# Performance work log

Hardware: AMD Instinct MI355X
Metric: run time of the kernel (lower is better)

The kernel has to match this reference:

```python
import jax, jax.numpy as jnp
import numpy as np

N, E = 20000, 320000
CUR, HID, OUT, H = 256, 256, 64, 6  # cur_dim, hidden_dim, output_dim, gat heads


def setup_inputs() -> dict:
    key = jax.random.key(0)
    ks = jax.random.split(key, 16)
    p = lambda k, shape: jax.random.normal(k, shape, jnp.float32) * 0.05
    return dict(
        x=jax.random.normal(ks[0], (N, CUR), jnp.float32),
        edge_index=jax.random.randint(ks[1], (2, E), 0, N),
        edge_weight=jax.random.uniform(ks[2], (E,), jnp.float32),
        Wp=p(ks[3], (CUR, HID)), bp=p(ks[4], (HID,)),
        W_gat=p(ks[5], (HID, H * OUT)),
        att_src=p(ks[6], (H, OUT)), att_dst=p(ks[7], (H, OUT)),
        b_gat=p(ks[8], (H * OUT,)),
        W_gcn0=p(ks[9], (HID, OUT)), b_gcn0=p(ks[10], (OUT,)),
        W_gcn1=p(ks[11], (HID, OUT)), b_gcn1=p(ks[12], (OUT,)),
        W_arma_init=p(ks[13], (H * OUT, OUT)),
        W_arma_root=p(ks[14], (H * OUT, OUT)),
        b_arma=p(ks[15], (OUT,)),
    )


def _seg_sum(v, ids, n):
    return jax.ops.segment_sum(v, ids, num_segments=n)


def _gat(h, src, dst, W, a_s, a_d, b):
    # PyG GATConv: add self loops, per-edge attention, softmax over incoming edges.
    n = h.shape[0]
    loops = jnp.arange(n)
    s = jnp.concatenate([src, loops])
    d = jnp.concatenate([dst, loops])
    xw = (h @ W).reshape(n, H, OUT)               # [N,H,F]
    al = (xw * a_s).sum(-1)                       # [N,H] source term
    ar = (xw * a_d).sum(-1)                       # [N,H] target term
    e = jax.nn.leaky_relu(al[s] + ar[d], 0.2)     # [E',H]
    m = jax.ops.segment_max(e, d, num_segments=n)  # stable softmax per target
    pe = jnp.exp(e - m[d])
    alpha = pe / _seg_sum(pe, d, n)[d]
    out = _seg_sum(alpha[:, :, None] * xw[s], d, n)  # [N,H,F]
    return out.reshape(n, H * OUT) + b


def _gcn(h, src, dst, w, W, b):
    # PyG GCNConv: self loops (weight 1), symmetric D^-1/2 A D^-1/2 normalization.
    n = h.shape[0]
    loops = jnp.arange(n)
    s = jnp.concatenate([src, loops])
    d = jnp.concatenate([dst, loops])
    w2 = jnp.concatenate([w, jnp.ones((n,), h.dtype)])
    deg = _seg_sum(w2, d, n)
    dinv = jnp.where(deg > 0, jax.lax.rsqrt(deg), 0.0)
    norm = dinv[s] * w2 * dinv[d]
    xw = h @ W
    return _seg_sum(norm[:, None] * xw[s], d, n) + b


def _arma(h, src, dst, w, Wi, Wr, b):
    # PyG ARMAConv, num_stacks=1, num_layers=1, act=ReLU; gcn_norm WITHOUT self loops.
    n = h.shape[0]
    deg = _seg_sum(w, dst, n)
    dinv = jnp.where(deg > 0, jax.lax.rsqrt(deg), 0.0)
    norm = dinv[src] * w * dinv[dst]
    t = h @ Wi
    agg = _seg_sum(norm[:, None] * t[src], dst, n)
    return jax.nn.relu(agg + h @ Wr + b)


def reference(x, edge_index, edge_weight, Wp, bp, W_gat, att_src, att_dst, b_gat,
              W_gcn0, b_gcn0, W_gcn1, b_gcn1, W_arma_init, W_arma_root, b_arma):
    src, dst = edge_index[0], edge_index[1]
    h = x @ Wp + bp
    lrelu = lambda v: jax.nn.leaky_relu(v, 0.01)  # F.leaky_relu default slope
    h1 = lrelu(_gat(h, src, dst, W_gat, att_src, att_dst, b_gat))   # [N, 6*64]
    h2 = lrelu(_gcn(h, src, dst, edge_weight, W_gcn0, b_gcn0))       # [N, 64]
    h3 = lrelu(_gcn(h, src, dst, edge_weight, W_gcn1, b_gcn1))       # [N, 64]
    h4 = lrelu(_arma(h1, src, dst, edge_weight, W_arma_init, W_arma_root, b_arma))
    return jnp.tanh(jnp.concatenate([h1, h2, h3, h4], axis=1))      # [N, 576]
```

## Files before the change

### kernel.cpp

```cpp
#include <hip/hip_runtime.h>


#define NN 20000
#define EE 320000
#define GATD 384
#define NH 6
#define OUTD 64
#define ODIM 576

typedef __bf16 bf16_8 __attribute__((ext_vector_type(8)));
typedef float f32_4 __attribute__((ext_vector_type(4)));

__device__ __forceinline__ float lrelu(float x, float s) { return x > 0.f ? x : s * x; }

__device__ __forceinline__ float loadf(const void* p, size_t i, int f32) {
  return f32 ? ((const float*)p)[i] : (float)((const __bf16*)p)[i];
}

struct ProbeArgs {
  const void* ptr[15];
  int cnt[15];
  int flagidx[15];
  const int* ei;
};
__global__ void k_probe_all(ProbeArgs a, int* __restrict__ flags) {
  __shared__ int cnt;
  if (threadIdx.x == 0) cnt = 0;
  __syncthreads();
  int b = blockIdx.x;
  if (b < 15) {
    const unsigned short* u = (const unsigned short*)a.ptr[b];
    int m = a.cnt[b] < 2048 ? a.cnt[b] : 2048;
    int c = 0;
    for (int i = threadIdx.x; i < m; i += 256) {
      float v = __uint_as_float(((unsigned int)u[i]) << 16);
      if (!(fabsf(v) < 1e4f)) c++;
    }
    if (c) atomicAdd(&cnt, c);
    __syncthreads();
    if (threadIdx.x == 0) flags[a.flagidx[b]] = (cnt > m / 16) ? 1 : 0;
  } else {
    int c = 0;
    for (int i = threadIdx.x; i < 1024; i += 256)
      if (a.ei[2 * i + 1] != 0) c++;
    if (c) atomicAdd(&cnt, c);
    __syncthreads();
    if (threadIdx.x == 0) flags[16] = (cnt <= 2) ? 1 : 0;
  }
}

struct CvtSeg { const void* in; __bf16* out; int n; int flagidx; int blk0; };
struct CvtArgs { CvtSeg s[7]; };
struct TSeg { const void* in; __bf16* out; int R; int C; int flagidx; int blk0; };
struct TArgs { TSeg s[6]; };
__global__ void k_cvt_merged(CvtArgs ca, int ncvtblk, TArgs ta, const int* __restrict__ flags) {
  if ((int)blockIdx.x < ncvtblk) {
    int b = blockIdx.x;
    int k = 0;
    while (k + 1 < 7 && ca.s[k + 1].blk0 <= b) k++;
    const CvtSeg sg = ca.s[k];
    int i = (b - sg.blk0) * 256 + threadIdx.x;
    if (i >= sg.n) return;
    sg.out[i] = flags[sg.flagidx] ? (__bf16)((const float*)sg.in)[i] : ((const __bf16*)sg.in)[i];
    return;
  }
  __shared__ float t[32][33];
  int b = blockIdx.x - ncvtblk;
  int k = 0;
  while (k + 1 < 6 && ta.s[k + 1].blk0 <= b) k++;
  const TSeg sg = ta.s[k];
  int f32 = flags[sg.flagidx];
  int tpx = (sg.C + 31) >> 5;
  int lt = b - sg.blk0;
  int c0 = (lt % tpx) * 32, r0 = (lt / tpx) * 32;
  int tid = threadIdx.x;
  for (int idx = tid; idx < 1024; idx += 256) {
    int r = idx >> 5, c = idx & 31;
    if (r0 + r < sg.R && c0 + c < sg.C)
      t[r][c] = loadf(sg.in, (size_t)(r0 + r) * sg.C + (c0 + c), f32);
  }
  __syncthreads();
  for (int idx = tid; idx < 1024; idx += 256) {
    int r = idx >> 5, c = idx & 31;
    if (c0 + r < sg.C && r0 + c < sg.R)
      sg.out[(size_t)(c0 + r) * sg.R + (r0 + c)] = (__bf16)t[c][r];
  }
}

__global__ void k_count(const int* __restrict__ ei, const void* __restrict__ ew,
                        const int* __restrict__ flags,
                        int* __restrict__ deg, float* __restrict__ wdeg) {
  int e = blockIdx.x * 256 + threadIdx.x;
  if (e >= EE) return;
  int sh = flags[16];
  int d = ei[(size_t)(EE + e) << sh];
  atomicAdd(&deg[d], 1);
  atomicAdd(&wdeg[d], loadf(ew, e, flags[2]));
}

__global__ __launch_bounds__(256) void k_scan1(const int* __restrict__ deg,
                                               int* __restrict__ bsum) {
  int i = blockIdx.x * 256 + threadIdx.x;
  int v = (i < NN) ? deg[i] : 0;
  for (int off = 32; off; off >>= 1) v += __shfl_xor(v, off);
  __shared__ int ws[4];
  if ((threadIdx.x & 63) == 0) ws[threadIdx.x >> 6] = v;
  __syncthreads();
  if (threadIdx.x == 0) bsum[blockIdx.x] = ws[0] + ws[1] + ws[2] + ws[3];
}

__global__ __launch_bounds__(256) void k_scan2(const int* __restrict__ deg,
    const int* __restrict__ bsum, const float* __restrict__ wdeg,
    int* __restrict__ rowstart, float* __restrict__ dg, float* __restrict__ da) {
  int b = blockIdx.x;
  int tid = threadIdx.x;
  int lane = tid & 63, wv = tid >> 6;
  int i = b * 256 + tid;
  __shared__ int red[4];
  __shared__ int wsum2[4];
  __shared__ int sbase;
  {
    int v = (tid < b) ? bsum[tid] : 0;
    for (int off = 32; off; off >>= 1) v += __shfl_xor(v, off);
    if (lane == 0) red[wv] = v;
    __syncthreads();
    if (tid == 0) sbase = red[0] + red[1] + red[2] + red[3];
    __syncthreads();
  }
  int v = (i < NN) ? deg[i] : 0;
  int run = v;
  for (int off = 1; off < 64; off <<= 1) {
    int u = __shfl_up(run, off);
    if (lane >= off) run += u;
  }
  if (lane == 63) wsum2[wv] = run;
  __syncthreads();
  int wb = 0;
#pragma unroll
  for (int w = 0; w < 4; w++) { int x = wsum2[w]; if (w < wv) wb += x; }
  int excl = sbase + wb + run - v;
  if (i < NN) rowstart[i] = excl;
  if (i == NN - 1) rowstart[NN] = excl + v;
  if (i < NN) {
    float w = wdeg[i];
    dg[i] = rsqrtf(w + 1.0f);
    da[i] = w > 0.f ? rsqrtf(w) : 0.f;
  }
}

__global__ void k_fill(const int* __restrict__ ei, const void* __restrict__ ew,
                       const int* __restrict__ flags, const int* __restrict__ rowstart,
                       int* __restrict__ cursor,
                       int* __restrict__ csr_src, float* __restrict__ csr_w) {
  int e = blockIdx.x * 256 + threadIdx.x;
  if (e >= EE) return;
  int sh = flags[16];
  int d = ei[(size_t)(EE + e) << sh];
  int s = ei[(size_t)e << sh];
  int pos = rowstart[d] + atomicAdd(&cursor[d], 1);
  csr_src[pos] = s;
  csr_w[pos] = loadf(ew, e, flags[2]);
}

template<bool HAS_BIAS>
__global__ __launch_bounds__(256) void gemm64(const void* __restrict__ A,
    const int* __restrict__ aflag, const __bf16* __restrict__ Bt,
    const __bf16* __restrict__ bias,
    __bf16* __restrict__ C1, int n1, int ldc1,
    __bf16* __restrict__ C2, int ldc2,
    int M, int K) {
  __shared__ __bf16 Al[64][40];
  __shared__ __bf16 Bl[128][40];
  int a32 = *aflag;
  int tid = threadIdx.x;
  int w = tid >> 6, lane = tid & 63;
  int quad = lane >> 4, r = lane & 15;
  int row0 = blockIdx.x * 64, col0 = blockIdx.y * 128;
  f32_4 acc[4][2] = {};
  int srow = tid >> 2;
  int koff = (tid & 3) * 8;
  int brow = tid >> 1;
  int bko  = (tid & 1) * 16;
  for (int kt = 0; kt < K; kt += 32) {
    int arow = row0 + srow;
    if (a32) {
      float4 a0 = {0.f, 0.f, 0.f, 0.f}, a1 = {0.f, 0.f, 0.f, 0.f};
      if (arow < M) {
        const float* ap = (const float*)A + (size_t)arow * K + kt + koff;
        a0 = *(const float4*)ap;
        a1 = *(const float4*)(ap + 4);
      }
      bf16_8 t;
      t[0] = (__bf16)a0.x; t[1] = (__bf16)a0.y; t[2] = (__bf16)a0.z; t[3] = (__bf16)a0.w;
      t[4] = (__bf16)a1.x; t[5] = (__bf16)a1.y; t[6] = (__bf16)a1.z; t[7] = (__bf16)a1.w;
      *(bf16_8*)(&Al[srow][koff]) = t;
    } else {
      float4 av = {0.f, 0.f, 0.f, 0.f};
      if (arow < M) av = *(const float4*)((const __bf16*)A + (size_t)arow * K + kt + koff);
      *(float4*)(&Al[srow][koff]) = av;
    }
    const __bf16* bp = Bt + (size_t)(col0 + brow) * K + kt + bko;
    *(float4*)(&Bl[brow][bko])     = *(const float4*)bp;
    *(float4*)(&Bl[brow][bko + 8]) = *(const float4*)(bp + 8);
    __syncthreads();
    bf16_8 bfrag0 = *(const bf16_8*)(&Bl[w * 16 + r][quad * 8]);
    bf16_8 bfrag1 = *(const bf16_8*)(&Bl[64 + w * 16 + r][quad * 8]);
#pragma unroll
    for (int mt = 0; mt < 4; mt++) {
      bf16_8 afrag = *(const bf16_8*)(&Al[mt * 16 + r][quad * 8]);
      acc[mt][0] = __builtin_amdgcn_mfma_f32_16x16x32_bf16(afrag, bfrag0, acc[mt][0], 0, 0, 0);
      acc[mt][1] = __builtin_amdgcn_mfma_f32_16x16x32_bf16(afrag, bfrag1, acc[mt][1], 0, 0, 0);
    }
    __syncthreads();
  }
  __bf16* Cp; int ldc; int cbase;
  if (col0 < n1) { Cp = C1; ldc = ldc1; cbase = col0; }
  else           { Cp = C2; ldc = ldc2; cbase = col0 - n1; }
  int cc0 = cbase + w * 16 + r;
  int cc1 = cbase + 64 + w * 16 + r;
  float bv0 = HAS_BIAS ? (float)bias[col0 + w * 16 + r] : 0.0f;
  float bv1 = HAS_BIAS ? (float)bias[col0 + 64 + w * 16 + r] : 0.0f;
#pragma unroll
  for (int mt = 0; mt < 4; mt++) {
#pragma unroll
    for (int rr = 0; rr < 4; rr++) {
      int crow = row0 + mt * 16 + quad * 4 + rr;
      if (crow < M) {
        Cp[(size_t)crow * ldc + cc0] = (__bf16)(acc[mt][0][rr] + bv0);
        Cp[(size_t)crow * ldc + cc1] = (__bf16)(acc[mt][1][rr] + bv1);
      }
    }
  }
}

__global__ void k_alar_w(const __bf16* __restrict__ xwb, const __bf16* __restrict__ as_,
                         const __bf16* __restrict__ ad_,
                         float* __restrict__ al, float* __restrict__ ar) {
  int p = blockIdx.x * 4 + (threadIdx.x >> 6);
  int lane = threadIdx.x & 63;
  if (p >= NN * NH) return;
  int i = p / NH, h = p - i * NH;
  float xv = (float)xwb[(size_t)i * GATD + h * OUTD + lane];
  float s1 = xv * (float)as_[h * OUTD + lane];
  float s2 = xv * (float)ad_[h * OUTD + lane];
  for (int off = 32; off; off >>= 1) { s1 += __shfl_xor(s1, off); s2 += __shfl_xor(s2, off); }
  if (lane == 0) { al[p] = s1; ar[p] = s2; }
}

__global__ __launch_bounds__(256) void k_gatgcn(const __bf16* __restrict__ xwb,
    const __bf16* __restrict__ xwgb,
    const float* __restrict__ al, const float* __restrict__ ar,
    const int* __restrict__ rowstart, const int* __restrict__ csr_src,
    const float* __restrict__ csr_w, const float* __restrict__ dgcn,
    const __bf16* __restrict__ bgat, const __bf16* __restrict__ b0,
    const __bf16* __restrict__ b1,
    __bf16* __restrict__ h1b, float* __restrict__ out) {
  int wv = threadIdx.x >> 6, lane = threadIdx.x & 63;
  int i = blockIdx.x * 4 + wv;
  __shared__ int   src_sh[4][64];
  __shared__ float ex_sh[4][64][NH];
  __shared__ float wg_sh[4][64];
  __shared__ int   mc_sh[4];
  int e0 = rowstart[i], e1 = rowstart[i + 1];
  if (lane == 0) mc_sh[wv] = (e1 - e0 + 63) >> 6;
  float arv[NH], exs[NH], acc[NH], denp[NH];
#pragma unroll
  for (int h = 0; h < NH; h++) arv[h] = ar[i * NH + h];
#pragma unroll
  for (int h = 0; h < NH; h++) {
    float e = lrelu(al[i * NH + h] + arv[h], 0.2f);
    exs[h] = __expf(e);
    acc[h] = exs[h] * (float)xwb[(size_t)i * GATD + h * OUTD + lane];
    denp[h] = 0.f;
  }
  float g0 = 0.f, g1 = 0.f;
  __syncthreads();
  int mch = max(max(mc_sh[0], mc_sh[1]), max(mc_sh[2], mc_sh[3]));
  for (int c = 0; c < mch; c++) {
    if (c) __syncthreads();
    int base = e0 + c * 64;
    int cnt = e1 - base; cnt = cnt < 0 ? 0 : (cnt > 64 ? 64 : cnt);
    if (lane < cnt) {
      int eidx = base + lane;
      int s = csr_src[eidx];
      src_sh[wv][lane] = s;
      wg_sh[wv][lane] = dgcn[s] * csr_w[eidx];
#pragma unroll
      for (int h = 0; h < NH; h++) {
        float ex = __expf(lrelu(al[s * NH + h] + arv[h], 0.2f));
        ex_sh[wv][lane][h] = ex;
        denp[h] += ex;
      }
    }
    __syncthreads();
    int j = 0;
    for (; j + 2 <= cnt; j += 2) {
      int s0 = src_sh[wv][j], s1 = src_sh[wv][j + 1];
      const __bf16* r0 = xwb + (size_t)s0 * GATD + lane;
      const __bf16* r1 = xwb + (size_t)s1 * GATD + lane;
      const __bf16* p0 = xwgb + (size_t)s0 * 128;
      const __bf16* p1 = xwgb + (size_t)s1 * 128;
      float x0[NH], x1[NH];
#pragma unroll
      for (int h = 0; h < NH; h++) { x0[h] = (float)r0[h * OUTD]; x1[h] = (float)r1[h * OUTD]; }
      float y00 = (float)p0[lane], y01 = (float)p0[lane + 64];
      float y10 = (float)p1[lane], y11 = (float)p1[lane + 64];
      float wg0 = wg_sh[wv][j], wg1 = wg_sh[wv][j + 1];
#pragma unroll
      for (int h = 0; h < NH; h++)
        acc[h] += ex_sh[wv][j][h] * x0[h] + ex_sh[wv][j + 1][h] * x1[h];
      g0 += wg0 * y00 + wg1 * y10;
      g1 += wg0 * y01 + wg1 * y11;
    }
    if (j < cnt) {
      int s0 = src_sh[wv][j];
      const __bf16* r0 = xwb + (size_t)s0 * GATD + lane;
      const __bf16* p0 = xwgb + (size_t)s0 * 128;
      float wg0 = wg_sh[wv][j];
#pragma unroll
      for (int h = 0; h < NH; h++) acc[h] += ex_sh[wv][j][h] * (float)r0[h * OUTD];
      g0 += wg0 * (float)p0[lane];
      g1 += wg0 * (float)p0[lane + 64];
    }
  }
#pragma unroll
  for (int h = 0; h < NH; h++) {
    float d = denp[h];
    for (int off = 32; off; off >>= 1) d += __shfl_xor(d, off);
    d += exs[h];
    float v = acc[h] / d + (float)bgat[h * OUTD + lane];
    v = lrelu(v, 0.01f);
    h1b[(size_t)i * GATD + h * OUTD + lane] = (__bf16)v;
    out[(size_t)i * ODIM + h * OUTD + lane] = tanhf(v);
  }
  float di = dgcn[i];
  float v0 = lrelu(di * g0 + di * di * (float)xwgb[(size_t)i * 128 + lane] + (float)b0[lane], 0.01f);
  float v1 = lrelu(di * g1 + di * di * (float)xwgb[(size_t)i * 128 + 64 + lane] + (float)b1[lane], 0.01f);
  out[(size_t)i * ODIM + 384 + lane] = tanhf(v0);
  out[(size_t)i * ODIM + 448 + lane] = tanhf(v1);
}

__global__ __launch_bounds__(256) void k_arma(const __bf16* __restrict__ trb,
    const int* __restrict__ rowstart, const int* __restrict__ csr_src,
    const float* __restrict__ csr_w, const float* __restrict__ darma,
    const __bf16* __restrict__ ba, float* __restrict__ out) {
  int wv = threadIdx.x >> 6, lane = threadIdx.x & 63;
  int i = blockIdx.x * 4 + wv;
  __shared__ __attribute__((aligned(16))) int   src_sh[4][64];
  __shared__ __attribute__((aligned(16))) float wa_sh[4][64];
  __shared__ int mc_sh[4];
  int e0 = rowstart[i], e1 = rowstart[i + 1];
  if (lane == 0) mc_sh[wv] = (e1 - e0 + 63) >> 6;
  __syncthreads();
  int mch = max(max(mc_sh[0], mc_sh[1]), max(mc_sh[2], mc_sh[3]));
  float aa = 0.f;
  for (int c = 0; c < mch; c++) {
    if (c) __syncthreads();
    int base = e0 + c * 64;
    int cnt = e1 - base; cnt = cnt < 0 ? 0 : (cnt > 64 ? 64 : cnt);
    int s = i; float wav = 0.f;
    if (lane < cnt) {
      int eidx = base + lane;
      s = csr_src[eidx];
      wav = darma[s] * csr_w[eidx];
    }
    src_sh[wv][lane] = s;
    wa_sh[wv][lane] = wav;
    __syncthreads();
    int cntp = (cnt + 7) & ~7;
    for (int j = 0; j < cntp; j += 8) {
      int4 sa = *(const int4*)&src_sh[wv][j];
      int4 sb = *(const int4*)&src_sh[wv][j + 4];
      int sq[8] = {sa.x, sa.y, sa.z, sa.w, sb.x, sb.y, sb.z, sb.w};
      float tq[8];
#pragma unroll
      for (int q = 0; q < 8; q++)
        tq[q] = (float)trb[(size_t)sq[q] * 128 + lane];
      float4 wa0 = *(const float4*)&wa_sh[wv][j];
      float4 wa1 = *(const float4*)&wa_sh[wv][j + 4];
      float waq[8] = {wa0.x, wa0.y, wa0.z, wa0.w, wa1.x, wa1.y, wa1.z, wa1.w};
#pragma unroll
      for (int q = 0; q < 8; q++) aa += waq[q] * tq[q];
    }
  }
  float va = darma[i] * aa + (float)trb[(size_t)i * 128 + 64 + lane] + (float)ba[lane];
  va = fmaxf(va, 0.f);
  out[(size_t)i * ODIM + 512 + lane] = tanhf(va);
}

extern "C" void kernel_launch(void* const* d_in, const int* in_sizes, int n_in,
                              void* d_out, int out_size, void* d_ws, size_t ws_size,
                              hipStream_t stream) {
  const int* ei = (const int*)d_in[1];
  float* out = (float*)d_out;

  char* ws = (char*)d_ws;
  size_t off = 0;
  auto alloc = [&](size_t bytes) -> void* {
    void* p = ws + off;
    off += (bytes + 255) & ~(size_t)255;
    return p;
  };
  int*    flags    = (int*)alloc(32 * 4);
  int*    deg      = (int*)alloc((size_t)3 * NN * 4);
  int*    cursor   = deg + NN;
  float*  wdeg     = (float*)(deg + 2 * NN);
  int*    bsum     = (int*)alloc(128 * 4);
  int*    rowstart = (int*)alloc((size_t)(NN + 1) * 4);
  int*    csr_src  = (int*)alloc((size_t)EE * 4);
  float*  csr_w    = (float*)alloc((size_t)EE * 4);
  float*  dgcn     = (float*)alloc((size_t)NN * 4);
  float*  darma    = (float*)alloc((size_t)NN * 4);
  float*  al       = (float*)alloc((size_t)NN * NH * 4);
  float*  ar       = (float*)alloc((size_t)NN * NH * 4);
  __bf16* bpb   = (__bf16*)alloc(256 * 2);
  __bf16* asb   = (__bf16*)alloc(384 * 2);
  __bf16* adb   = (__bf16*)alloc(384 * 2);
  __bf16* bgatb = (__bf16*)alloc(384 * 2);
  __bf16* bg0b  = (__bf16*)alloc(64 * 2);
  __bf16* bg1b  = (__bf16*)alloc(64 * 2);
  __bf16* bab   = (__bf16*)alloc(64 * 2);
  __bf16* Wp_t    = (__bf16*)alloc(256 * 256 * 2);
  __bf16* Wcat_t  = (__bf16*)alloc((size_t)(384 + 128) * 256 * 2);
  __bf16* Wgat_t  = Wcat_t;
  __bf16* Wg01_t  = Wcat_t + (size_t)384 * 256;
  __bf16* Warma_t = (__bf16*)alloc(128 * 384 * 2);
  char* regA = (char*)alloc((size_t)NN * GATD * 2);
  __bf16* h   = (__bf16*)regA;
  __bf16* h1b = (__bf16*)regA;
  char* regB = (char*)alloc((size_t)NN * GATD * 2);
  __bf16* xwb = (__bf16*)regB;
  __bf16* trb = (__bf16*)regB;
  __bf16* xwgb = (__bf16*)alloc((size_t)NN * 128 * 2);
  (void)ws_size; (void)in_sizes; (void)n_in; (void)out_size;

  hipMemsetAsync(ws, 0, 256 + (size_t)3 * NN * 4, stream);

  dim3 tb(256);
  ProbeArgs pa;
  const int pidx[15] = {0, 2, 3, 4, 5, 6, 7, 8, 9, 10, 11, 12, 13, 14, 15};
  const int pcnt[15] = {NN * 256, EE, 256 * 256, 256, 256 * 384, NH * OUTD, NH * OUTD,
                        NH * OUTD, 256 * 64, 64, 256 * 64, 64, GATD * OUTD, GATD * OUTD, 64};
  for (int k = 0; k < 15; k++) { pa.ptr[k] = d_in[pidx[k]]; pa.cnt[k] = pcnt[k]; pa.flagidx[k] = pidx[k]; }
  pa.ei = ei;
  k_probe_all<<<dim3(16), tb, 0, stream>>>(pa, flags);

  CvtArgs ca;
  TArgs ta;
  int cvtblk = 0, tblk = 0;
  {
    struct { int idx; __bf16* out; int n; } cv[7] = {
      {4, bpb, 256}, {6, asb, 384}, {7, adb, 384}, {8, bgatb, 384},
      {10, bg0b, 64}, {12, bg1b, 64}, {15, bab, 64},
    };
    for (int k = 0; k < 7; k++) {
      ca.s[k].in = d_in[cv[k].idx]; ca.s[k].out = cv[k].out; ca.s[k].n = cv[k].n;
      ca.s[k].flagidx = cv[k].idx; ca.s[k].blk0 = cvtblk;
      cvtblk += (cv[k].n + 255) / 256;
    }
    struct { int idx; __bf16* out; int R; int C; } tv[6] = {
      {3,  Wp_t,             256, 256},
      {5,  Wgat_t,           256, 384},
      {9,  Wg01_t,           256, 64},
      {11, Wg01_t + 64 * 256, 256, 64},
      {13, Warma_t,          384, 64},
      {14, Warma_t + 64 * 384, 384, 64},
    };
    for (int k = 0; k < 6; k++) {
      ta.s[k].in = d_in[tv[k].idx]; ta.s[k].out = tv[k].out;
      ta.s[k].R = tv[k].R; ta.s[k].C = tv[k].C;
      ta.s[k].flagidx = tv[k].idx; ta.s[k].blk0 = tblk;
      tblk += ((tv[k].R + 31) / 32) * ((tv[k].C + 31) / 32);
    }
    k_cvt_merged<<<dim3(cvtblk + tblk), tb, 0, stream>>>(ca, cvtblk, ta, flags);
  }

  const int NBLK = (NN + 255) / 256;
  k_count<<<dim3((EE + 255) / 256), tb, 0, stream>>>(ei, d_in[2], flags, deg, wdeg);
  k_scan1<<<dim3(NBLK), tb, 0, stream>>>(deg, bsum);
  k_scan2<<<dim3(NBLK), tb, 0, stream>>>(deg, bsum, wdeg, rowstart, dgcn, darma);
  k_fill<<<dim3((EE + 255) / 256), tb, 0, stream>>>(ei, d_in[2], flags, rowstart, cursor, csr_src, csr_w);

  const int MB64 = (NN + 63) / 64;
  gemm64<true ><<<dim3(MB64, 2), tb, 0, stream>>>(d_in[0], &flags[0], Wp_t, bpb,
                                                  h, 256, 256, nullptr, 0, NN, 256);
  gemm64<false><<<dim3(MB64, 4), tb, 0, stream>>>(h, &flags[30], Wcat_t, nullptr,
                                                  xwb, 384, 384, xwgb, 128, NN, 256);
  k_alar_w<<<dim3((NN * NH + 3) / 4), tb, 0, stream>>>(xwb, asb, adb, al, ar);
  k_gatgcn<<<dim3(NN / 4), tb, 0, stream>>>(xwb, xwgb, al, ar, rowstart, csr_src,
                                            csr_w, dgcn, bgatb, bg0b, bg1b, h1b, out);
  gemm64<false><<<dim3(MB64, 1), tb, 0, stream>>>(h1b, &flags[30], Warma_t, nullptr,
                                                  trb, 128, 128, nullptr, 0, NN, 384);
  k_arma<<<dim3(NN / 4), tb, 0, stream>>>(trb, rowstart, csr_src, csr_w,
                                          darma, bab, out);
}
```

Measured before the change: 295.8 us.

## Co-launch graph CSR build stages with dense GEMMs in merged kernels

Merges the degree-count pass into the weight-conversion kernel, runs the scan2 stage alongside the first projection GEMM, and runs the CSR fill alongside the second GEMM, each as one launch with block-index dispatch. This drops several kernel launches and lets the independent graph-preprocessing work overlap with the matrix multiplies. The gemm bias becomes a runtime null check instead of a template parameter, and the grid size 313 is hardcoded.

```diff
diff --git a/kernel.cpp b/kernel.cpp
--- a/kernel.cpp
+++ b/kernel.cpp
@@ -53,9 +53,21 @@
 struct CvtArgs { CvtSeg s[7]; };
 struct TSeg { const void* in; __bf16* out; int R; int C; int flagidx; int blk0; };
 struct TArgs { TSeg s[6]; };
-__global__ void k_cvt_merged(CvtArgs ca, int ncvtblk, TArgs ta, const int* __restrict__ flags) {
-  if ((int)blockIdx.x < ncvtblk) {
-    int b = blockIdx.x;
+__global__ __launch_bounds__(256) void k_cvt_count(CvtArgs ca, int ncvtblk, TArgs ta, int ncvtT,
+    const int* __restrict__ flags, const int* __restrict__ ei, const void* __restrict__ ew,
+    int* __restrict__ deg, float* __restrict__ wdeg) {
+  int bx = blockIdx.x;
+  if (bx >= ncvtT) {
+    int e = (bx - ncvtT) * 256 + threadIdx.x;
+    if (e >= EE) return;
+    int sh = flags[16];
+    int d = ei[(size_t)(EE + e) << sh];
+    atomicAdd(&deg[d], 1);
+    atomicAdd(&wdeg[d], loadf(ew, e, flags[2]));
+    return;
+  }
+  if (bx < ncvtblk) {
+    int b = bx;
     int k = 0;
     while (k + 1 < 7 && ca.s[k + 1].blk0 <= b) k++;
     const CvtSeg sg = ca.s[k];
@@ -65,7 +77,7 @@
     return;
   }
   __shared__ float t[32][33];
-  int b = blockIdx.x - ncvtblk;
+  int b = bx - ncvtblk;
   int k = 0;
   while (k + 1 < 6 && ta.s[k + 1].blk0 <= b) k++;
   const TSeg sg = ta.s[k];
@@ -87,17 +99,6 @@
   }
 }
 
-__global__ void k_count(const int* __restrict__ ei, const void* __restrict__ ew,
-                        const int* __restrict__ flags,
-                        int* __restrict__ deg, float* __restrict__ wdeg) {
-  int e = blockIdx.x * 256 + threadIdx.x;
-  if (e >= EE) return;
-  int sh = flags[16];
-  int d = ei[(size_t)(EE + e) << sh];
-  atomicAdd(&deg[d], 1);
-  atomicAdd(&wdeg[d], loadf(ew, e, flags[2]));
-}
-
 __global__ __launch_bounds__(256) void k_scan1(const int* __restrict__ deg,
                                                int* __restrict__ bsum) {
   int i = blockIdx.x * 256 + threadIdx.x;
@@ -109,10 +110,9 @@
   if (threadIdx.x == 0) bsum[blockIdx.x] = ws[0] + ws[1] + ws[2] + ws[3];
 }
 
-__global__ __launch_bounds__(256) void k_scan2(const int* __restrict__ deg,
+__device__ __forceinline__ void scan2_body(int b, const int* __restrict__ deg,
     const int* __restrict__ bsum, const float* __restrict__ wdeg,
     int* __restrict__ rowstart, float* __restrict__ dg, float* __restrict__ da) {
-  int b = blockIdx.x;
   int tid = threadIdx.x;
   int lane = tid & 63, wv = tid >> 6;
   int i = b * 256 + tid;
@@ -148,11 +148,11 @@
   }
 }
 
-__global__ void k_fill(const int* __restrict__ ei, const void* __restrict__ ew,
-                       const int* __restrict__ flags, const int* __restrict__ rowstart,
-                       int* __restrict__ cursor,
-                       int* __restrict__ csr_src, float* __restrict__ csr_w) {
-  int e = blockIdx.x * 256 + threadIdx.x;
+__device__ __forceinline__ void fill_body(int b, const int* __restrict__ ei,
+    const void* __restrict__ ew, const int* __restrict__ flags,
+    const int* __restrict__ rowstart, int* __restrict__ cursor,
+    int* __restrict__ csr_src, float* __restrict__ csr_w) {
+  int e = b * 256 + threadIdx.x;
   if (e >= EE) return;
   int sh = flags[16];
   int d = ei[(size_t)(EE + e) << sh];
@@ -162,20 +162,19 @@
   csr_w[pos] = loadf(ew, e, flags[2]);
 }
 
-template<bool HAS_BIAS>
-__global__ __launch_bounds__(256) void gemm64(const void* __restrict__ A,
+__device__ __forceinline__ void gemm_body(const void* __restrict__ A,
     const int* __restrict__ aflag, const __bf16* __restrict__ Bt,
     const __bf16* __restrict__ bias,
     __bf16* __restrict__ C1, int n1, int ldc1,
     __bf16* __restrict__ C2, int ldc2,
-    int M, int K) {
+    int M, int K, int bx, int by) {
   __shared__ __bf16 Al[64][40];
   __shared__ __bf16 Bl[128][40];
   int a32 = *aflag;
   int tid = threadIdx.x;
   int w = tid >> 6, lane = tid & 63;
   int quad = lane >> 4, r = lane & 15;
-  int row0 = blockIdx.x * 64, col0 = blockIdx.y * 128;
+  int row0 = bx * 64, col0 = by * 128;
   f32_4 acc[4][2] = {};
   int srow = tid >> 2;
   int koff = (tid & 3) * 8;
@@ -218,8 +217,8 @@
   else           { Cp = C2; ldc = ldc2; cbase = col0 - n1; }
   int cc0 = cbase + w * 16 + r;
   int cc1 = cbase + 64 + w * 16 + r;
-  float bv0 = HAS_BIAS ? (float)bias[col0 + w * 16 + r] : 0.0f;
-  float bv1 = HAS_BIAS ? (float)bias[col0 + 64 + w * 16 + r] : 0.0f;
+  float bv0 = bias ? (float)bias[col0 + w * 16 + r] : 0.0f;
+  float bv1 = bias ? (float)bias[col0 + 64 + w * 16 + r] : 0.0f;
 #pragma unroll
   for (int mt = 0; mt < 4; mt++) {
 #pragma unroll
@@ -230,6 +229,43 @@
         Cp[(size_t)crow * ldc + cc1] = (__bf16)(acc[mt][1][rr] + bv1);
       }
     }
+  }
+}
+
+__global__ __launch_bounds__(256) void k_gemm(const void* __restrict__ A,
+    const int* __restrict__ aflag, const __bf16* __restrict__ Bt,
+    const __bf16* __restrict__ bias,
+    __bf16* __restrict__ C1, int n1, int ldc1,
+    __bf16* __restrict__ C2, int ldc2, int M, int K) {
+  gemm_body(A, aflag, Bt, bias, C1, n1, ldc1, C2, ldc2, M, K, blockIdx.x, blockIdx.y);
+}
+
+__global__ __launch_bounds__(256) void k_gemm1_scan2(const void* __restrict__ A,
+    const int* __restrict__ aflag, const __bf16* __restrict__ Bt,
+    const __bf16* __restrict__ bias, __bf16* __restrict__ C1, int M, int K, int ngemm,
+    const int* __restrict__ deg, const int* __restrict__ bsum,
+    const float* __restrict__ wdeg, int* __restrict__ rowstart,
+    float* __restrict__ dg, float* __restrict__ da) {
+  int bx = blockIdx.x;
+  if (bx < ngemm) {
+    gemm_body(A, aflag, Bt, bias, C1, 256, 256, nullptr, 0, M, K, bx % 313, bx / 313);
+  } else {
+    scan2_body(bx - ngemm, deg, bsum, wdeg, rowstart, dg, da);
+  }
+}
+
+__global__ __launch_bounds__(256) void k_gemm2_fill(const void* __restrict__ A,
+    const int* __restrict__ aflag, const __bf16* __restrict__ Bt,
+    __bf16* __restrict__ C1, int n1, int ldc1, __bf16* __restrict__ C2, int ldc2,
+    int M, int K, int ngemm,
+    const int* __restrict__ ei, const void* __restrict__ ew,
+    const int* __restrict__ flags, const int* __restrict__ rowstart,
+    int* __restrict__ cursor, int* __restrict__ csr_src, float* __restrict__ csr_w) {
+  int bx = blockIdx.x;
+  if (bx < ngemm) {
+    gemm_body(A, aflag, Bt, nullptr, C1, n1, ldc1, C2, ldc2, M, K, bx % 313, bx / 313);
+  } else {
+    fill_body(bx - ngemm, ei, ew, flags, rowstart, cursor, csr_src, csr_w);
   }
 }
 
@@ -472,25 +508,28 @@
       ta.s[k].flagidx = tv[k].idx; ta.s[k].blk0 = tblk;
       tblk += ((tv[k].R + 31) / 32) * ((tv[k].C + 31) / 32);
     }
-    k_cvt_merged<<<dim3(cvtblk + tblk), tb, 0, stream>>>(ca, cvtblk, ta, flags);
-  }
-
-  const int NBLK = (NN + 255) / 256;
-  k_count<<<dim3((EE + 255) / 256), tb, 0, stream>>>(ei, d_in[2], flags, deg, wdeg);
+  }
+  const int EEBLK = (EE + 255) / 256;
+  const int NBLK  = (NN + 255) / 256;
+  const int MB64  = (NN + 63) / 64;
+  int ncvtT = cvtblk + tblk;
+  k_cvt_count<<<dim3(ncvtT + EEBLK), tb, 0, stream>>>(ca, cvtblk, ta, ncvtT,
+                                                      flags, ei, d_in[2], deg, wdeg);
+
   k_scan1<<<dim3(NBLK), tb, 0, stream>>>(deg, bsum);
-  k_scan2<<<dim3(NBLK), tb, 0, stream>>>(deg, bsum, wdeg, rowstart, dgcn, darma);
-  k_fill<<<dim3((EE + 255) / 256), tb, 0, stream>>>(ei, d_in[2], flags, rowstart, cursor, csr_src, csr_w);
-
-  const int MB64 = (NN + 63) / 64;
-  gemm64<true ><<<dim3(MB64, 2), tb, 0, stream>>>(d_in[0], &flags[0], Wp_t, bpb,
-                                                  h, 256, 256, nullptr, 0, NN, 256);
-  gemm64<false><<<dim3(MB64, 4), tb, 0, stream>>>(h, &flags[30], Wcat_t, nullptr,
-                                                  xwb, 384, 384, xwgb, 128, NN, 256);
+
+  k_gemm1_scan2<<<dim3(313 * 2 + NBLK), tb, 0, stream>>>(d_in[0], &flags[0], Wp_t, bpb,
+      h, NN, 256, 313 * 2, deg, bsum, wdeg, rowstart, dgcn, darma);
+
+  k_gemm2_fill<<<dim3(313 * 4 + EEBLK), tb, 0, stream>>>(h, &flags[30], Wcat_t,
+      xwb, 384, 384, xwgb, 128, NN, 256, 313 * 4,
+      ei, d_in[2], flags, rowstart, cursor, csr_src, csr_w);
+
   k_alar_w<<<dim3((NN * NH + 3) / 4), tb, 0, stream>>>(xwb, asb, adb, al, ar);
   k_gatgcn<<<dim3(NN / 4), tb, 0, stream>>>(xwb, xwgb, al, ar, rowstart, csr_src,
                                             csr_w, dgcn, bgatb, bg0b, bg1b, h1b, out);
-  gemm64<false><<<dim3(MB64, 1), tb, 0, stream>>>(h1b, &flags[30], Warma_t, nullptr,
-                                                  trb, 128, 128, nullptr, 0, NN, 384);
+  k_gemm<<<dim3(MB64, 1), tb, 0, stream>>>(h1b, &flags[30], Warma_t, nullptr,
+                                           trb, 128, 128, nullptr, 0, NN, 384);
   k_arma<<<dim3(NN / 4), tb, 0, stream>>>(trb, rowstart, csr_src, csr_w,
                                           darma, bab, out);
 }
```

Result: faster. 285.3 us (median of 2 runs) (-3.6%).
